# Kernel optimization log

Hardware: AMD Instinct MI355X
Metric: run time of the kernel (lower is better)

The kernel has to match this reference:

```python
import jax, jax.numpy as jnp
import numpy as np

VOCAB = 512
EMB = 256
HID = 64
T_HORIZON = 0.05


def setup_inputs() -> dict:
    key = jax.random.key(0)
    ks = jax.random.split(key, 6)
    B, L = 32, 4096
    x = jax.random.randint(ks[0], (B, L), 0, VOCAB, dtype=jnp.int64 if jax.config.jax_enable_x64 else jnp.int32)
    emb_table = jax.random.normal(ks[1], (VOCAB, EMB), dtype=jnp.float32)
    W1 = jax.random.normal(ks[2], (EMB, HID), dtype=jnp.float32) * (1.0 / np.sqrt(EMB))
    b1 = jnp.zeros((HID,), dtype=jnp.float32)
    W2 = jax.random.normal(ks[3], (HID, VOCAB), dtype=jnp.float32) * (1.0 / np.sqrt(HID))
    b2 = jnp.full((VOCAB,), 0.1, dtype=jnp.float32)  # torch: bias.data.fill_(0.1)
    return {"x": x, "emb_table": emb_table, "W1": W1, "b1": b1, "W2": W2, "b2": b2, "steps": 5}


def reference(x, emb_table, W1, b1, W2, b2, steps):
    """Vectorized Gillespie-style Markov jump simulation.

    Equivalent to the torch loop: intensity is computed once per step from the
    current state, then every (b, l) position samples a candidate next state
    from softmax(intensity) with the self-transition zeroed and renormalized
    (== categorical over logits with the current state masked to -inf), and
    accepts it with prob 1 - exp(-rate * dt).
    """
    V = emb_table.shape[0]
    dt = T_HORIZON / steps
    key = jax.random.key(42)
    keys = jax.random.split(key, steps)
    vocab_ids = jnp.arange(V)

    def step(x_t, k):
        # intensity: [B, L, V]
        h = jax.nn.relu(emb_table[x_t] @ W1 + b1)
        intensity = h @ W2 + b2
        # mask self-transition (softmax * (1 - onehot) then renormalize)
        self_mask = x_t[..., None] == vocab_ids  # [B, L, V] bool
        masked_logits = jnp.where(self_mask, -jnp.inf, intensity)
        k1, k2 = jax.random.split(k)
        next_state = jax.random.categorical(k1, masked_logits)  # [B, L]
        rate = jnp.take_along_axis(intensity, next_state[..., None], axis=-1)[..., 0]
        accept_prob = 1.0 - jnp.exp(-rate * dt)
        u = jax.random.uniform(k2, x_t.shape, dtype=rate.dtype)
        x_t = jnp.where(u < accept_prob, next_state.astype(x_t.dtype), x_t)
        return x_t, None

    x_final, _ = jax.lax.scan(step, x, keys)
    return x_final
```

## Files before the change

### kernel.cpp

```cpp
#include <hip/hip_runtime.h>
#include <stdint.h>


#define VOCAB 512
#define EMB   256
#define HID   64
#define NPOS  (32 * 4096)
#define STEPS 5
#define PPW   8
#define NWAVES (NPOS / PPW)

__host__ __device__ __forceinline__ void tf2x32(uint32_t k0, uint32_t k1,
                                                uint32_t x0, uint32_t x1,
                                                uint32_t& o0, uint32_t& o1) {
  uint32_t ks2 = k0 ^ k1 ^ 0x1BD11BDAu;
  x0 += k0; x1 += k1;
#define TFR(r) { x0 += x1; x1 = (x1 << (r)) | (x1 >> (32 - (r))); x1 ^= x0; }
  TFR(13) TFR(15) TFR(26) TFR(6)
  x0 += k1;  x1 += ks2 + 1u;
  TFR(17) TFR(29) TFR(16) TFR(24)
  x0 += ks2; x1 += k0 + 2u;
  TFR(13) TFR(15) TFR(26) TFR(6)
  x0 += k0;  x1 += k1 + 3u;
  TFR(17) TFR(29) TFR(16) TFR(24)
  x0 += k1;  x1 += ks2 + 4u;
  TFR(13) TFR(15) TFR(26) TFR(6)
  x0 += ks2; x1 += k0 + 5u;
#undef TFR
  o0 = x0; o1 = x1;
}

struct Keys {
  uint32_t k1a[STEPS], k1b[STEPS];
  uint32_t k2a[STEPS], k2b[STEPS];
};

__global__ __launch_bounds__(256)
void build_h(const float* __restrict__ emb,
             const float* __restrict__ W1,
             const float* __restrict__ b1,
             float* __restrict__ H) {
  const int s   = blockIdx.x;
  const int hid = threadIdx.x & (HID - 1);
  const int kq  = threadIdx.x >> 6;
  const float* e = emb + s * EMB;
  double acc = 0.0;
#pragma unroll 4
  for (int k = kq; k < EMB; k += 4)
    acc += (double)e[k] * (double)W1[k * HID + hid];
  __shared__ double part[4][HID];
  part[kq][hid] = acc;
  __syncthreads();
  if (kq == 0) {
    const double a = (part[0][hid] + part[1][hid]) + (part[2][hid] + part[3][hid]);
    const float m = (float)a + b1[hid];
    H[s * HID + hid] = m > 0.0f ? m : 0.0f;
  }
}

__global__ __launch_bounds__(256)
void build_table2(const float* __restrict__ W2,
                  const float* __restrict__ b2,
                  const float* __restrict__ H,
                  float* __restrict__ I,
                  float* __restrict__ pthr) {
  const int s   = blockIdx.x;
  const int tid = threadIdx.x;
  __shared__ float h[HID];
  __shared__ float redmax[4];
  if (tid < HID) h[tid] = H[s * HID + tid];
  __syncthreads();
  double acc0 = 0.0, acc1 = 0.0;
#pragma unroll 8
  for (int k = 0; k < HID; ++k) {
    const float hk = h[k];
    acc0 += (double)hk * (double)W2[k * VOCAB + tid];
    acc1 += (double)hk * (double)W2[k * VOCAB + tid + 256];
  }
  const float v0 = (float)acc0 + b2[tid];
  const float v1 = (float)acc1 + b2[tid + 256];
  I[s * VOCAB + tid]       = v0;
  I[s * VOCAB + tid + 256] = v1;
  float lmax = fmaxf(v0, v1);
  for (int off = 32; off > 0; off >>= 1)
    lmax = fmaxf(lmax, __shfl_xor(lmax, off, 64));
  if ((tid & 63) == 0) redmax[tid >> 6] = lmax;
  __syncthreads();
  if (tid == 0) {
    const float m = fmaxf(fmaxf(redmax[0], redmax[1]), fmaxf(redmax[2], redmax[3]));
    const float z = (-m) * 0.01f;
    pthr[s] = 1.0f - (float)exp((double)z);
  }
}

__global__ __launch_bounds__(256)
void markov_kernel(const int* __restrict__ x_in,
                   const float* __restrict__ I,
                   const float* __restrict__ pthr,
                   int* __restrict__ x_out,
                   Keys K) {
  __shared__ float sp[VOCAB];
  sp[threadIdx.x]       = pthr[threadIdx.x];
  sp[threadIdx.x + 256] = pthr[threadIdx.x + 256];
  __syncthreads();

  const int gtid = blockIdx.x * blockDim.x + threadIdx.x;
  const int wave = gtid >> 6;
  const int lane = gtid & 63;
  const int base = wave * PPW;
  const float TINYF = 1.17549435e-38f;

  float r0 = 0.0f;
  if (lane < PPW * STEPS) {
    const int p = lane / 5, t = lane % 5;
    uint32_t w0, w1;
    tf2x32(K.k2a[t], K.k2b[t], 0u, (uint32_t)(base + p), w0, w1);
    r0 = __uint_as_float((((w0 ^ w1) >> 9) | 0x3f800000u)) - 1.0f;
  }
  const int sload = (lane < PPW) ? x_in[base + lane] : 0;
  int result = 0;

#pragma unroll
  for (int p = 0; p < PPW; ++p) {
    int s = __shfl(sload, p, 64);
    s = __builtin_amdgcn_readfirstlane(s);
#pragma unroll
    for (int t = 0; t < STEPS; ++t) {
      const float u = __shfl(r0, p * STEPS + t, 64);
      if (u >= sp[s]) continue;

      const float* row = I + s * VOCAB;
      float best = -__builtin_inff();
      int bidx = 0;
      const uint32_t fbase = ((uint32_t)(base + p) << 9) + (uint32_t)lane;
#pragma unroll
      for (int j = 0; j < VOCAB / 64; ++j) {
        const int v = lane + (j << 6);
        uint32_t w0, w1;
        tf2x32(K.k1a[t], K.k1b[t], 0u, fbase + ((uint32_t)j << 6), w0, w1);
        const uint32_t bits = w0 ^ w1;
        float uf = __uint_as_float((bits >> 9) | 0x3f800000u) - 1.0f;
        if (uf == 0.0f) uf = TINYF;
        const float g = -logf(-logf(uf));
        if (v != s) {
          const float val = row[v] + g;
          if (val > best) { best = val; bidx = v; }
        }
      }
      for (int off = 32; off > 0; off >>= 1) {
        const float ob = __shfl_xor(best, off, 64);
        const int   oi = __shfl_xor(bidx, off, 64);
        if (ob > best || (ob == best && oi < bidx)) { best = ob; bidx = oi; }
      }
      bidx = __builtin_amdgcn_readfirstlane(bidx);
      const float rate = row[bidx];
      const float z = (-rate) * 0.01f;
      const float pacc = 1.0f - (float)exp((double)z);
      if (u < pacc) { s = bidx; }
    }
    result = (lane == p) ? s : result;
  }
  if (lane < PPW) x_out[base + lane] = result;
}

extern "C" void kernel_launch(void* const* d_in, const int* in_sizes, int n_in,
                              void* d_out, int out_size, void* d_ws, size_t ws_size,
                              hipStream_t stream) {
  const int*   x   = (const int*)d_in[0];
  const float* emb = (const float*)d_in[1];
  const float* W1  = (const float*)d_in[2];
  const float* b1  = (const float*)d_in[3];
  const float* W2  = (const float*)d_in[4];
  const float* b2  = (const float*)d_in[5];
  float* I    = (float*)d_ws;
  float* pthr = (float*)d_ws + VOCAB * VOCAB;
  float* H    = pthr + VOCAB;
  int* out = (int*)d_out;

  Keys K;
  for (int t = 0; t < STEPS; ++t) {
    uint32_t Sa, Sb;
    tf2x32(0u, 42u, 0u, (uint32_t)t, Sa, Sb);
    tf2x32(Sa, Sb, 0u, 0u, K.k1a[t], K.k1b[t]);
    tf2x32(Sa, Sb, 0u, 1u, K.k2a[t], K.k2b[t]);
  }

  build_h<<<VOCAB, 256, 0, stream>>>(emb, W1, b1, H);
  build_table2<<<VOCAB, 256, 0, stream>>>(W2, b2, H, I, pthr);
  markov_kernel<<<(NWAVES * 64) / 256, 256, 0, stream>>>(x, I, pthr, out, K);
}
```

Measured before the change: 125.6 us.

## Fuse table-building kernels and iterate only over candidate jump steps via ballot mask

The two precompute kernels become one 512-thread kernel that keeps the hidden vector in shared memory, which drops one launch and the global round trip for H. The Markov kernel no longer loops over all position/step pairs with per-iteration checks. It builds a wavefront ballot mask of (position, step) pairs whose uniform draw falls below the state's acceptance threshold and visits only those. After an accepted jump it recomputes the mask for that position's later steps using the new state's threshold. This removes serialized uniform-branch overhead, but adds ballot and bookkeeping logic and relies on the threshold bound being exact.

```diff
diff --git a/kernel.cpp b/kernel.cpp
--- a/kernel.cpp
+++ b/kernel.cpp
@@ -35,59 +35,53 @@
   uint32_t k2a[STEPS], k2b[STEPS];
 };
 
-__global__ __launch_bounds__(256)
-void build_h(const float* __restrict__ emb,
-             const float* __restrict__ W1,
-             const float* __restrict__ b1,
-             float* __restrict__ H) {
+__global__ __launch_bounds__(512)
+void build_table(const float* __restrict__ emb,
+                 const float* __restrict__ W1,
+                 const float* __restrict__ b1,
+                 const float* __restrict__ W2,
+                 const float* __restrict__ b2,
+                 float* __restrict__ I,
+                 float* __restrict__ pthr) {
   const int s   = blockIdx.x;
-  const int hid = threadIdx.x & (HID - 1);
-  const int kq  = threadIdx.x >> 6;
+  const int tid = threadIdx.x;
+  __shared__ double part[8][HID];
+  __shared__ double hd[HID];
+  __shared__ float  redmax[8];
+
+  const int hid = tid & (HID - 1);
+  const int kq  = tid >> 6;
   const float* e = emb + s * EMB;
   double acc = 0.0;
-#pragma unroll 4
-  for (int k = kq; k < EMB; k += 4)
+#pragma unroll
+  for (int k = kq; k < EMB; k += 8)
     acc += (double)e[k] * (double)W1[k * HID + hid];
-  __shared__ double part[4][HID];
   part[kq][hid] = acc;
   __syncthreads();
   if (kq == 0) {
-    const double a = (part[0][hid] + part[1][hid]) + (part[2][hid] + part[3][hid]);
+    const double a = ((part[0][hid] + part[1][hid]) + (part[2][hid] + part[3][hid]))
+                   + ((part[4][hid] + part[5][hid]) + (part[6][hid] + part[7][hid]));
     const float m = (float)a + b1[hid];
-    H[s * HID + hid] = m > 0.0f ? m : 0.0f;
+    hd[hid] = (double)(m > 0.0f ? m : 0.0f);
   }
-}
+  __syncthreads();
 
-__global__ __launch_bounds__(256)
-void build_table2(const float* __restrict__ W2,
-                  const float* __restrict__ b2,
-                  const float* __restrict__ H,
-                  float* __restrict__ I,
-                  float* __restrict__ pthr) {
-  const int s   = blockIdx.x;
-  const int tid = threadIdx.x;
-  __shared__ float h[HID];
-  __shared__ float redmax[4];
-  if (tid < HID) h[tid] = H[s * HID + tid];
-  __syncthreads();
-  double acc0 = 0.0, acc1 = 0.0;
-#pragma unroll 8
-  for (int k = 0; k < HID; ++k) {
-    const float hk = h[k];
-    acc0 += (double)hk * (double)W2[k * VOCAB + tid];
-    acc1 += (double)hk * (double)W2[k * VOCAB + tid + 256];
-  }
-  const float v0 = (float)acc0 + b2[tid];
-  const float v1 = (float)acc1 + b2[tid + 256];
-  I[s * VOCAB + tid]       = v0;
-  I[s * VOCAB + tid + 256] = v1;
-  float lmax = fmaxf(v0, v1);
+  double acc2 = 0.0;
+#pragma unroll
+  for (int k = 0; k < HID; ++k)
+    acc2 += hd[k] * (double)W2[k * VOCAB + tid];
+  const float val = (float)acc2 + b2[tid];
+  I[s * VOCAB + tid] = val;
+
+  float lmax = val;
   for (int off = 32; off > 0; off >>= 1)
     lmax = fmaxf(lmax, __shfl_xor(lmax, off, 64));
   if ((tid & 63) == 0) redmax[tid >> 6] = lmax;
   __syncthreads();
   if (tid == 0) {
-    const float m = fmaxf(fmaxf(redmax[0], redmax[1]), fmaxf(redmax[2], redmax[3]));
+    float m = redmax[0];
+#pragma unroll
+    for (int i = 1; i < 8; ++i) m = fmaxf(m, redmax[i]);
     const float z = (-m) * 0.01f;
     pthr[s] = 1.0f - (float)exp((double)z);
   }
@@ -110,57 +104,65 @@
   const int base = wave * PPW;
   const float TINYF = 1.17549435e-38f;
 
-  float r0 = 0.0f;
+  const int qp = lane / 5;
+  const int qt = lane - qp * 5;
+  float u40 = 0.0f;
   if (lane < PPW * STEPS) {
-    const int p = lane / 5, t = lane % 5;
     uint32_t w0, w1;
-    tf2x32(K.k2a[t], K.k2b[t], 0u, (uint32_t)(base + p), w0, w1);
-    r0 = __uint_as_float((((w0 ^ w1) >> 9) | 0x3f800000u)) - 1.0f;
+    tf2x32(K.k2a[qt], K.k2b[qt], 0u, (uint32_t)(base + qp), w0, w1);
+    u40 = __uint_as_float((((w0 ^ w1) >> 9) | 0x3f800000u)) - 1.0f;
   }
-  const int sload = (lane < PPW) ? x_in[base + lane] : 0;
-  int result = 0;
+  int scur = (lane < PPW) ? x_in[base + lane] : 0;
 
+  const int s_of_q = __shfl(scur, qp, 64);
+  const bool cand = (lane < PPW * STEPS) && (u40 < sp[s_of_q]);
+  unsigned long long mask = __ballot(cand);
+
+  while (mask) {
+    const int q = (int)__builtin_ctzll(mask);
+    mask &= mask - 1;
+    const int p = q / 5;
+    const int t = q - p * 5;
+    const int s = __builtin_amdgcn_readfirstlane(__shfl(scur, p, 64));
+
+    const float* row = I + s * VOCAB;
+    float best = -__builtin_inff();
+    int bidx = 0;
+    const uint32_t fbase = ((uint32_t)(base + p) << 9) + (uint32_t)lane;
 #pragma unroll
-  for (int p = 0; p < PPW; ++p) {
-    int s = __shfl(sload, p, 64);
-    s = __builtin_amdgcn_readfirstlane(s);
-#pragma unroll
-    for (int t = 0; t < STEPS; ++t) {
-      const float u = __shfl(r0, p * STEPS + t, 64);
-      if (u >= sp[s]) continue;
-
-      const float* row = I + s * VOCAB;
-      float best = -__builtin_inff();
-      int bidx = 0;
-      const uint32_t fbase = ((uint32_t)(base + p) << 9) + (uint32_t)lane;
-#pragma unroll
-      for (int j = 0; j < VOCAB / 64; ++j) {
-        const int v = lane + (j << 6);
-        uint32_t w0, w1;
-        tf2x32(K.k1a[t], K.k1b[t], 0u, fbase + ((uint32_t)j << 6), w0, w1);
-        const uint32_t bits = w0 ^ w1;
-        float uf = __uint_as_float((bits >> 9) | 0x3f800000u) - 1.0f;
-        if (uf == 0.0f) uf = TINYF;
-        const float g = -logf(-logf(uf));
-        if (v != s) {
-          const float val = row[v] + g;
-          if (val > best) { best = val; bidx = v; }
-        }
+    for (int j = 0; j < VOCAB / 64; ++j) {
+      const int v = lane + (j << 6);
+      uint32_t w0, w1;
+      tf2x32(K.k1a[t], K.k1b[t], 0u, fbase + ((uint32_t)j << 6), w0, w1);
+      const uint32_t bits = w0 ^ w1;
+      float uf = __uint_as_float((bits >> 9) | 0x3f800000u) - 1.0f;
+      if (uf == 0.0f) uf = TINYF;
+      const float g = -logf(-logf(uf));
+      if (v != s) {
+        const float val = row[v] + g;
+        if (val > best) { best = val; bidx = v; }
       }
-      for (int off = 32; off > 0; off >>= 1) {
-        const float ob = __shfl_xor(best, off, 64);
-        const int   oi = __shfl_xor(bidx, off, 64);
-        if (ob > best || (ob == best && oi < bidx)) { best = ob; bidx = oi; }
-      }
-      bidx = __builtin_amdgcn_readfirstlane(bidx);
-      const float rate = row[bidx];
-      const float z = (-rate) * 0.01f;
-      const float pacc = 1.0f - (float)exp((double)z);
-      if (u < pacc) { s = bidx; }
     }
-    result = (lane == p) ? s : result;
+    for (int off = 32; off > 0; off >>= 1) {
+      const float ob = __shfl_xor(best, off, 64);
+      const int   oi = __shfl_xor(bidx, off, 64);
+      if (ob > best || (ob == best && oi < bidx)) { best = ob; bidx = oi; }
+    }
+    bidx = __builtin_amdgcn_readfirstlane(bidx);
+    const float rate = row[bidx];
+    const float z = (-rate) * 0.01f;
+    const float pacc = 1.0f - (float)exp((double)z);
+    const float u = __shfl(u40, q, 64);
+    if (u < pacc) {
+      if (lane == p) scur = bidx;
+      const unsigned long long fut =
+          (((1ull << (p * 5 + 5)) - 1) & ~((1ull << (q + 1)) - 1));
+      const float pnew = sp[bidx];
+      const unsigned long long nb = __ballot(u40 < pnew) & fut;
+      mask = (mask & ~fut) | nb;
+    }
   }
-  if (lane < PPW) x_out[base + lane] = result;
+  if (lane < PPW) x_out[base + lane] = scur;
 }
 
 extern "C" void kernel_launch(void* const* d_in, const int* in_sizes, int n_in,
@@ -174,7 +176,6 @@
   const float* b2  = (const float*)d_in[5];
   float* I    = (float*)d_ws;
   float* pthr = (float*)d_ws + VOCAB * VOCAB;
-  float* H    = pthr + VOCAB;
   int* out = (int*)d_out;
 
   Keys K;
@@ -185,7 +186,6 @@
     tf2x32(Sa, Sb, 0u, 1u, K.k2a[t], K.k2b[t]);
   }
 
-  build_h<<<VOCAB, 256, 0, stream>>>(emb, W1, b1, H);
-  build_table2<<<VOCAB, 256, 0, stream>>>(W2, b2, H, I, pthr);
+  build_table<<<VOCAB, 512, 0, stream>>>(emb, W1, b1, W2, b2, I, pthr);
   markov_kernel<<<(NWAVES * 64) / 256, 256, 0, stream>>>(x, I, pthr, out, K);
 }
```

Result: faster. 121.5 us (-3.3%).
